# Kernel optimization log

Measured on AMD Instinct MI355X. Metric: run time of the kernel, lower is better.

Reference implementation:

```python
import jax, jax.numpy as jnp
import numpy as np

N_ITEMS = 30000
D = 128            # embedding_dim
F = D // 2 + 1     # freq_dim = 65
RAW_IMG = 1024
RAW_TXT = 768


def setup_inputs() -> dict:
    key = jax.random.key(0)
    ks = jax.random.split(key, 13)
    return {
        "image_embeds": jax.random.normal(ks[0], (N_ITEMS, D), jnp.float32),
        "text_embeds": jax.random.normal(ks[1], (N_ITEMS, D), jnp.float32),
        "image_table": jax.random.normal(ks[2], (N_ITEMS, RAW_IMG), jnp.float32),
        "text_table": jax.random.normal(ks[3], (N_ITEMS, RAW_TXT), jnp.float32),
        "W_img": jax.random.normal(ks[4], (RAW_IMG, D), jnp.float32) * 0.02,
        "b_img": jax.random.normal(ks[5], (D,), jnp.float32) * 0.02,
        "W_txt": jax.random.normal(ks[6], (RAW_TXT, D), jnp.float32) * 0.02,
        "b_txt": jax.random.normal(ks[7], (D,), jnp.float32) * 0.02,
        "avrf_img": jax.random.normal(ks[8], (F,), jnp.float32),
        "avrf_txt": jax.random.normal(ks[9], (F,), jnp.float32),
        "avg_R": jax.random.normal(ks[10], (F,), jnp.float32),
        "psi": jax.random.normal(ks[11], (F,), jnp.float32) * 0.1,
        "lambda_weights": jnp.array([0.6, 0.4], jnp.float32),
    }


def reference(image_embeds, text_embeds, image_table, text_table,
              W_img, b_img, W_txt, b_txt,
              avrf_img, avrf_txt, avg_R, psi, lambda_weights):
    # project full embedding tables: [N, raw] @ [raw, D] -> [N, D]
    proj_image = image_table @ W_img + b_img
    proj_txt = text_table @ W_txt + b_txt
    # per-row rFFT -> [N, F] complex
    img_fft = jnp.fft.rfft(proj_image, axis=1, norm="ortho")
    txt_fft = jnp.fft.rfft(proj_txt, axis=1, norm="ortho")
    # phase alignment rotation
    phi = avg_R * 0.5 + psi                      # [F]
    rot = jnp.exp(-1j * phi.astype(jnp.complex64))
    APC_img = img_fft * rot[None, :]
    APC_txt = txt_fft * jnp.conj(rot)[None, :]
    # AVRF (variance-ratio) masking -- torch forward uses the raw logit params
    img_vr = APC_img * avrf_img[None, :]
    txt_vr = APC_txt * avrf_txt[None, :]
    # IMCF: magnitude-squared coherence masking
    cross = APC_img * jnp.conj(APC_txt)
    msc = jnp.abs(cross) ** 2 / (jnp.abs(APC_img) ** 2 * jnp.abs(APC_txt) ** 2 + 1e-8)
    img_imcf = APC_img * msc
    txt_imcf = APC_txt * msc
    # softmax-weighted late fusion of the two filtered spectra
    lam = jax.nn.softmax(lambda_weights)
    img_late = lam[0] * img_vr + lam[1] * img_imcf
    txt_late = lam[0] * txt_vr + lam[1] * txt_imcf
    image_conv = jnp.fft.irfft(img_late, n=image_embeds.shape[1], axis=1, norm="ortho")
    text_conv = jnp.fft.irfft(txt_late, n=text_embeds.shape[1], axis=1, norm="ortho")
    return image_conv, text_conv
```

## Files before the change

kernel.cpp:

```cpp
#include <hip/hip_runtime.h>
#include <math.h>

typedef __bf16 bf16x8 __attribute__((ext_vector_type(8)));
typedef float f32x4 __attribute__((ext_vector_type(4)));
typedef unsigned short ushort_t;

#define BM 64
#define KS 32
#define S128 0.08838834764831845f
#define TWOPI_128 0.04908738521234052f

__device__ __align__(16) ushort_t g_wft[(32 + 24) * 2 * 6144];
__device__ __align__(16) ushort_t g_gt[6 * 2 * 4096];
__device__ float g_fp[96 * 8];
__device__ unsigned g_spill[512 * 12288];

__device__ __forceinline__ void split2(float v, ushort_t& h, ushort_t& l) {
  unsigned u = __float_as_uint(v);
  h = (ushort_t)(u >> 16);
  float hf = __uint_as_float(u & 0xFFFF0000u);
  float lo = v - hf;
  unsigned ul = __float_as_uint(lo);
  l = (ushort_t)((ul + 0x7FFFu + ((ul >> 16) & 1u)) >> 16);
}

__device__ __forceinline__ void gll16(const void* gsrc, void* ldst) {
  __builtin_amdgcn_global_load_lds(
      (const __attribute__((address_space(1))) unsigned int*)gsrc,
      (__attribute__((address_space(3))) unsigned int*)ldst, 16, 0, 0);
}

__global__ void k_setup_wft(const float* __restrict__ Wimg,
                            const float* __restrict__ Wtxt, int Kimg, int Ktxt) {
  int gid = blockIdx.x * 256 + threadIdx.x;
  int imgn = Kimg * 192;
  if (gid >= imgn + Ktxt * 192) return;
  const float* W;
  int k, c;
  ushort_t* base;
  if (gid < imgn) {
    k = gid / 192; c = gid % 192; W = Wimg + (size_t)k * 128; base = g_wft;
  } else {
    int l = gid - imgn;
    k = l / 192; c = l % 192; W = Wtxt + (size_t)k * 128;
    base = g_wft + (size_t)(Kimg / 32) * 12288;
  }
  int grp = c >> 5, wi = c & 31, part = wi >> 4, fl = grp * 16 + (wi & 15);
  float val = 0.f;
  if (fl <= 64) {
    float re = 0.f, im = 0.f;
    float sts, stc;
    sincosf(TWOPI_128 * (float)fl, &sts, &stc);
    for (int d0 = 0; d0 < 128; d0 += 16) {
      int m = (fl * d0) & 127;
      float sa, ca;
      sincosf(TWOPI_128 * (float)m, &sa, &ca);
      float cr = ca, ci = -sa;
#pragma unroll
      for (int j = 0; j < 16; ++j) {
        float w = W[d0 + j];
        re = fmaf(w, cr, re);
        im = fmaf(w, ci, im);
        float nc = cr * stc + ci * sts;
        ci = ci * stc - cr * sts;
        cr = nc;
      }
    }
    val = (part == 0 ? re : im) * S128;
  }
  ushort_t h, l;
  split2(val, h, l);
  int ks = k >> 5, kin = k & 31;
  base[(size_t)(ks * 2 + 0) * 6144 + c * 32 + kin] = h;
  base[(size_t)(ks * 2 + 1) * 6144 + c * 32 + kin] = l;
}

__global__ void k_setup_gt(void) {
  int gid = blockIdx.x * 256 + threadIdx.x;
  if (gid >= 192 * 128) return;
  int pk = gid >> 7, n = gid & 127;
  int grp = pk >> 5, wi = pk & 31, part = wi >> 4, fl = grp * 16 + (wi & 15);
  float val = 0.f;
  if (fl <= 64) {
    float ck = (fl == 0 || fl == 64) ? 1.f : 2.f;
    int m = (fl * n) & 127;
    float sa, ca;
    sincosf(TWOPI_128 * (float)m, &sa, &ca);
    val = (part == 0 ? ca : -sa) * ck * S128;
  }
  ushort_t h, l;
  split2(val, h, l);
  g_gt[(size_t)(grp * 2 + 0) * 4096 + n * 32 + wi] = h;
  g_gt[(size_t)(grp * 2 + 1) * 4096 + n * 32 + wi] = l;
}

__global__ void k_setup_fp(const float* __restrict__ b_img, const float* __restrict__ b_txt,
                           const float* __restrict__ avrf_img, const float* __restrict__ avrf_txt,
                           const float* __restrict__ avg_R, const float* __restrict__ psi) {
  int gid = blockIdx.x * 256 + threadIdx.x;
  if (gid >= 96 * 4) return;
  int k = gid >> 2, q = gid & 3;
  float* fp = g_fp + k * 8;
  if (k > 64) {
    if (q == 0) { fp[0] = 1.f; fp[1] = 0.f; fp[2] = 0.f; fp[3] = 0.f; }
    fp[4 + q] = 0.f;
    return;
  }
  if (q == 0) {
    float phi = avg_R[k] * 0.5f + psi[k];
    float s, c;
    sincosf(phi, &s, &c);
    fp[0] = c; fp[1] = s; fp[2] = avrf_img[k]; fp[3] = avrf_txt[k];
  }
  const float* b = (q < 2) ? b_img : b_txt;
  int part = q & 1;
  float acc = 0.f;
  for (int d = 0; d < 128; ++d) {
    int m = (k * d) & 127;
    float sa, ca;
    sincosf(TWOPI_128 * (float)m, &sa, &ca);
    acc = fmaf(b[d], part ? -sa : ca, acc);
  }
  fp[4 + q] = acc * S128;
}

__global__ __launch_bounds__(256, 2) void fused_kernel(
    const float* __restrict__ Aimg, const float* __restrict__ Atxt,
    const float* __restrict__ lamw, float* __restrict__ out,
    int M, int Kimg, int Ktxt) {
  __shared__ __align__(16) char smem[67584];
  float* A_lds = (float*)smem;
  ushort_t* B_lds = (ushort_t*)(smem + 16384);
  ushort_t* Yhi = (ushort_t*)smem;
  ushort_t* Ylo = (ushort_t*)(smem + 25600);
  ushort_t* G_lds = (ushort_t*)(smem + 51200);

  const int tid = threadIdx.x, blk = blockIdx.x;
  const int lane = tid & 63, wv = tid >> 6;
  const int la = lane & 15, hh = lane >> 4;
  const int wr = wv >> 1, wc = wv & 1;
  const int row0 = blk * BM;

  f32x4 acc[2][6];

  auto stageA = [&](const float* A, int K, int s, int buf) {
#pragma unroll
    for (int i = 0; i < 2; ++i) {
      int idx = i * 256 + tid;
      int r = idx >> 3, sl = idx & 7;
      int kg = sl ^ (r & 7);
      int grow = row0 + r;
      if (grow > M - 1) grow = M - 1;
      const float* src = A + (size_t)grow * K + s * KS + kg * 4;
      char* dst = (char*)A_lds + buf * 8192 + i * 4096 + wv * 1024;
      gll16(src, dst);
    }
  };
  auto stageB = [&](const ushort_t* wft, int s, int buf) {
#pragma unroll
    for (int i = 0; i < 6; ++i) {
      const ushort_t* src = wft + (size_t)s * 12288 + i * 2048 + tid * 8;
      char* dst = (char*)B_lds + buf * 24576 + i * 4096 + wv * 1024;
      gll16(src, dst);
    }
  };

  auto gemm = [&](const float* A, int K, const ushort_t* wft) {
#pragma unroll
    for (int rt = 0; rt < 2; ++rt)
#pragma unroll
      for (int ct = 0; ct < 6; ++ct) acc[rt][ct] = (f32x4){0.f, 0.f, 0.f, 0.f};
    const int nst = K / KS;
    stageA(A, K, 0, 0);
    stageB(wft, 0, 0);
    for (int s = 0; s < nst; ++s) {
      const int cur = s & 1;
      __syncthreads();
      if (s + 1 < nst) { stageA(A, K, s + 1, cur ^ 1); stageB(wft, s + 1, cur ^ 1); }
      bf16x8 fah[2], fal[2];
#pragma unroll
      for (int rt = 0; rt < 2; ++rt) {
        int row = wr * 32 + rt * 16 + la;
        const float* ab = A_lds + cur * 2048 + row * 32;
        int s0 = (2 * hh) ^ (row & 7);
        int s1 = s0 ^ 1;
        f32x4 q0 = *(const f32x4*)(ab + s0 * 4);
        f32x4 q1 = *(const f32x4*)(ab + s1 * 4);
        ushort_t h8[8], l8[8];
#pragma unroll
        for (int j = 0; j < 4; ++j) {
          split2(q0[j], h8[j], l8[j]);
          split2(q1[j], h8[4 + j], l8[4 + j]);
        }
        fah[rt] = *(bf16x8*)h8;
        fal[rt] = *(bf16x8*)l8;
      }
#pragma unroll
      for (int ct = 0; ct < 6; ++ct) {
        int pcol = wc * 96 + ct * 16 + la;
        const ushort_t* bb = B_lds + cur * 12288 + pcol * 32 + hh * 8;
        bf16x8 fbh = *(const bf16x8*)bb;
        bf16x8 fbl = *(const bf16x8*)(bb + 6144);
#pragma unroll
        for (int rt = 0; rt < 2; ++rt) {
          acc[rt][ct] = __builtin_amdgcn_mfma_f32_16x16x32_bf16(fah[rt], fbh, acc[rt][ct], 0, 0, 0);
          acc[rt][ct] = __builtin_amdgcn_mfma_f32_16x16x32_bf16(fah[rt], fbl, acc[rt][ct], 0, 0, 0);
          acc[rt][ct] = __builtin_amdgcn_mfma_f32_16x16x32_bf16(fal[rt], fbh, acc[rt][ct], 0, 0, 0);
        }
      }
    }
  };

  auto idft = [&](float* outp) {
    f32x4 acc2[2][4];
#pragma unroll
    for (int rt = 0; rt < 2; ++rt)
#pragma unroll
      for (int ct = 0; ct < 4; ++ct) acc2[rt][ct] = (f32x4){0.f, 0.f, 0.f, 0.f};
    for (int ks = 0; ks < 6; ++ks) {
      __syncthreads();
#pragma unroll
      for (int i = 0; i < 4; ++i) {
        const ushort_t* src = g_gt + (size_t)ks * 8192 + i * 2048 + tid * 8;
        char* dst = (char*)G_lds + i * 4096 + wv * 1024;
        gll16(src, dst);
      }
      __syncthreads();
      bf16x8 yah[2], yal[2];
#pragma unroll
      for (int rt = 0; rt < 2; ++rt) {
        int row = wr * 32 + rt * 16 + la;
        int yb = row * 200 + ks * 32 + hh * 8;
        yah[rt] = *(const bf16x8*)&Yhi[yb];
        yal[rt] = *(const bf16x8*)&Ylo[yb];
      }
#pragma unroll
      for (int ct = 0; ct < 4; ++ct) {
        int col = wc * 64 + ct * 16 + la;
        const ushort_t* gb = G_lds + col * 32 + hh * 8;
        bf16x8 gbh = *(const bf16x8*)gb;
        bf16x8 gbl = *(const bf16x8*)(gb + 4096);
#pragma unroll
        for (int rt = 0; rt < 2; ++rt) {
          acc2[rt][ct] = __builtin_amdgcn_mfma_f32_16x16x32_bf16(yah[rt], gbh, acc2[rt][ct], 0, 0, 0);
          acc2[rt][ct] = __builtin_amdgcn_mfma_f32_16x16x32_bf16(yah[rt], gbl, acc2[rt][ct], 0, 0, 0);
          acc2[rt][ct] = __builtin_amdgcn_mfma_f32_16x16x32_bf16(yal[rt], gbh, acc2[rt][ct], 0, 0, 0);
        }
      }
    }
#pragma unroll
    for (int rt = 0; rt < 2; ++rt)
#pragma unroll
      for (int ct = 0; ct < 4; ++ct)
#pragma unroll
        for (int j = 0; j < 4; ++j) {
          int row = row0 + wr * 32 + rt * 16 + hh * 4 + j;
          if (row < M) outp[(size_t)row * 128 + wc * 64 + ct * 16 + la] = acc2[rt][ct][j];
        }
  };

  gemm(Aimg, Kimg, g_wft);
#pragma unroll
  for (int rt = 0; rt < 2; ++rt)
#pragma unroll
    for (int ct = 0; ct < 6; ++ct)
#pragma unroll
      for (int j = 0; j < 4; ++j) {
        ushort_t h, l;
        split2(acc[rt][ct][j], h, l);
        g_spill[(size_t)blk * 12288 + ((rt * 6 + ct) * 4 + j) * 256 + tid] =
            ((unsigned)h << 16) | l;
      }
  gemm(Atxt, Ktxt, g_wft + (size_t)(Kimg / 32) * 12288);
  __syncthreads();

  float l0 = lamw[0], l1 = lamw[1];
  float mx = fmaxf(l0, l1);
  float e0 = expf(l0 - mx), e1 = expf(l1 - mx);
  float lam0 = e0 / (e0 + e1), lam1 = e1 / (e0 + e1);
#pragma unroll
  for (int rt = 0; rt < 2; ++rt)
#pragma unroll
    for (int g = 0; g < 3; ++g) {
      int k = (wc * 3 + g) * 16 + la;
      const float* fp = g_fp + k * 8;
      float rc = fp[0], rs = fp[1], avI = fp[2], avT = fp[3];
      float bIr = fp[4], bIi = fp[5], bTr = fp[6], bTi = fp[7];
#pragma unroll
      for (int j = 0; j < 4; ++j) {
        unsigned uir = g_spill[(size_t)blk * 12288 + ((rt * 6 + 2 * g) * 4 + j) * 256 + tid];
        unsigned uii = g_spill[(size_t)blk * 12288 + ((rt * 6 + 2 * g + 1) * 4 + j) * 256 + tid];
        float Sir = __uint_as_float(uir & 0xFFFF0000u) + __uint_as_float(uir << 16) + bIr;
        float Sii = __uint_as_float(uii & 0xFFFF0000u) + __uint_as_float(uii << 16) + bIi;
        float Str = acc[rt][2 * g][j] + bTr;
        float Sti = acc[rt][2 * g + 1][j] + bTi;
        float Air = Sir * rc + Sii * rs, Aii = Sii * rc - Sir * rs;
        float Atr = Str * rc - Sti * rs, Ati = Sti * rc + Str * rs;
        float cre = Air * Atr + Aii * Ati, cim = Aii * Atr - Air * Ati;
        float pa = Air * Air + Aii * Aii, pb = Atr * Atr + Ati * Ati;
        float msc = (cre * cre + cim * cim) / (pa * pb + 1e-8f);
        float mi = lam0 * avI + lam1 * msc, mt = lam0 * avT + lam1 * msc;
        int row = wr * 32 + rt * 16 + hh * 4 + j;
        int pc = (wc * 3 + g) * 32 + la;
        ushort_t yh, yl;
        split2(Air * mi, yh, yl); Yhi[row * 200 + pc] = yh; Ylo[row * 200 + pc] = yl;
        split2(Aii * mi, yh, yl); Yhi[row * 200 + pc + 16] = yh; Ylo[row * 200 + pc + 16] = yl;
        acc[rt][2 * g][j] = Atr * mt;
        acc[rt][2 * g + 1][j] = Ati * mt;
      }
    }

  idft(out);
  __syncthreads();
#pragma unroll
  for (int rt = 0; rt < 2; ++rt)
#pragma unroll
    for (int g = 0; g < 3; ++g)
#pragma unroll
      for (int j = 0; j < 4; ++j) {
        int row = wr * 32 + rt * 16 + hh * 4 + j;
        int pc = (wc * 3 + g) * 32 + la;
        ushort_t yh, yl;
        split2(acc[rt][2 * g][j], yh, yl);
        Yhi[row * 200 + pc] = yh; Ylo[row * 200 + pc] = yl;
        split2(acc[rt][2 * g + 1][j], yh, yl);
        Yhi[row * 200 + pc + 16] = yh; Ylo[row * 200 + pc + 16] = yl;
      }
  idft(out + (size_t)M * 128);
}

extern "C" void kernel_launch(void* const* d_in, const int* in_sizes, int n_in,
                              void* d_out, int out_size, void* d_ws, size_t ws_size,
                              hipStream_t stream) {
  const float* image_table = (const float*)d_in[2];
  const float* text_table  = (const float*)d_in[3];
  const float* W_img = (const float*)d_in[4];
  const float* b_img = (const float*)d_in[5];
  const float* W_txt = (const float*)d_in[6];
  const float* b_txt = (const float*)d_in[7];
  const float* avrf_img = (const float*)d_in[8];
  const float* avrf_txt = (const float*)d_in[9];
  const float* avg_R = (const float*)d_in[10];
  const float* psi = (const float*)d_in[11];
  const float* lamw = (const float*)d_in[12];

  const int M = in_sizes[0] / 128;
  const int K_img = in_sizes[4] / 128;
  const int K_txt = in_sizes[6] / 128;

  int wft_threads = (K_img + K_txt) * 192;
  k_setup_wft<<<(wft_threads + 255) / 256, 256, 0, stream>>>(W_img, W_txt, K_img, K_txt);
  k_setup_gt<<<(192 * 128 + 255) / 256, 256, 0, stream>>>();
  k_setup_fp<<<2, 256, 0, stream>>>(b_img, b_txt, avrf_img, avrf_txt, avg_R, psi);
  fused_kernel<<<(M + BM - 1) / BM, 256, 0, stream>>>(
      image_table, text_table, lamw, (float*)d_out, M, K_img, K_txt);
}
```

Baseline: 133.6 us.

## Split fused kernel into per-modality GEMM and separate iDFT/filter kernel

Replaces the single fused kernel, which ran image and text GEMMs back to back per block, with a GEMM kernel that launches separate blocks for each modality. This doubles the grid and raises parallelism. The GEMM pre-splits A into bf16 hi/lo once at LDS write time rather than per fragment read. It also changes the weight and iDFT-matrix layouts to 8-element granules and stores the biased spectra to a global buffer. A second kernel reloads both spectra, applies the phase rotation and masks, and runs the inverse DFT for both outputs. The cost is an extra global round trip for the spectra and an extra launch, and the GEMM loop drops LDS double buffering.

```diff
diff --git a/kernel.cpp b/kernel.cpp
--- a/kernel.cpp
+++ b/kernel.cpp
@@ -3,25 +3,25 @@
 
 typedef __bf16 bf16x8 __attribute__((ext_vector_type(8)));
 typedef float f32x4 __attribute__((ext_vector_type(4)));
-typedef unsigned short ushort_t;
-
-#define BM 64
-#define KS 32
+typedef unsigned short u16;
+typedef unsigned int u32;
+
 #define S128 0.08838834764831845f
 #define TWOPI_128 0.04908738521234052f
-
-__device__ __align__(16) ushort_t g_wft[(32 + 24) * 2 * 6144];
-__device__ __align__(16) ushort_t g_gt[6 * 2 * 4096];
-__device__ float g_fp[96 * 8];
-__device__ unsigned g_spill[512 * 12288];
-
-__device__ __forceinline__ void split2(float v, ushort_t& h, ushort_t& l) {
+#define MROWS 30016
+
+__device__ __align__(16) u16 g_wft[56 * 12288];
+__device__ __align__(16) u16 g_gt[6 * 8192];
+__device__ __align__(16) float g_fp[96 * 8];
+__device__ __align__(16) u32 g_S[(size_t)2 * 6 * 4 * MROWS * 8];
+
+__device__ __forceinline__ void split2(float v, u16& h, u16& l) {
   unsigned u = __float_as_uint(v);
-  h = (ushort_t)(u >> 16);
+  h = (u16)(u >> 16);
   float hf = __uint_as_float(u & 0xFFFF0000u);
   float lo = v - hf;
   unsigned ul = __float_as_uint(lo);
-  l = (ushort_t)((ul + 0x7FFFu + ((ul >> 16) & 1u)) >> 16);
+  l = (u16)((ul + 0x7FFFu + ((ul >> 16) & 1u)) >> 16);
 }
 
 __device__ __forceinline__ void gll16(const void* gsrc, void* ldst) {
@@ -33,53 +33,63 @@
 __global__ void k_setup_wft(const float* __restrict__ Wimg,
                             const float* __restrict__ Wtxt, int Kimg, int Ktxt) {
   int gid = blockIdx.x * 256 + threadIdx.x;
-  int imgn = Kimg * 192;
-  if (gid >= imgn + Ktxt * 192) return;
-  const float* W;
-  int k, c;
-  ushort_t* base;
+  int imgn = Kimg * 96;
+  if (gid >= imgn + Ktxt * 96) return;
+  const float* Wrow;
+  u16* base;
+  int kloc, fq;
   if (gid < imgn) {
-    k = gid / 192; c = gid % 192; W = Wimg + (size_t)k * 128; base = g_wft;
+    kloc = gid / 96; fq = gid % 96;
+    Wrow = Wimg + (size_t)kloc * 128;
+    base = g_wft + (size_t)(kloc >> 5) * 12288;
   } else {
     int l = gid - imgn;
-    k = l / 192; c = l % 192; W = Wtxt + (size_t)k * 128;
-    base = g_wft + (size_t)(Kimg / 32) * 12288;
-  }
-  int grp = c >> 5, wi = c & 31, part = wi >> 4, fl = grp * 16 + (wi & 15);
-  float val = 0.f;
-  if (fl <= 64) {
-    float re = 0.f, im = 0.f;
+    kloc = l / 96; fq = l % 96;
+    Wrow = Wtxt + (size_t)kloc * 128;
+    base = g_wft + (size_t)(32 + (kloc >> 5)) * 12288;
+  }
+  float re = 0.f, im = 0.f;
+  if (fq <= 64) {
     float sts, stc;
-    sincosf(TWOPI_128 * (float)fl, &sts, &stc);
+    sincosf(TWOPI_128 * (float)fq, &sts, &stc);
     for (int d0 = 0; d0 < 128; d0 += 16) {
-      int m = (fl * d0) & 127;
+      int m = (fq * d0) & 127;
       float sa, ca;
       sincosf(TWOPI_128 * (float)m, &sa, &ca);
       float cr = ca, ci = -sa;
-#pragma unroll
-      for (int j = 0; j < 16; ++j) {
-        float w = W[d0 + j];
-        re = fmaf(w, cr, re);
-        im = fmaf(w, ci, im);
+      float wv[16];
+      *(float4*)&wv[0]  = *(const float4*)&Wrow[d0];
+      *(float4*)&wv[4]  = *(const float4*)&Wrow[d0 + 4];
+      *(float4*)&wv[8]  = *(const float4*)&Wrow[d0 + 8];
+      *(float4*)&wv[12] = *(const float4*)&Wrow[d0 + 12];
+#pragma unroll
+      for (int jj = 0; jj < 16; ++jj) {
+        re = fmaf(wv[jj], cr, re);
+        im = fmaf(wv[jj], ci, im);
         float nc = cr * stc + ci * sts;
         ci = ci * stc - cr * sts;
         cr = nc;
       }
     }
-    val = (part == 0 ? re : im) * S128;
-  }
-  ushort_t h, l;
-  split2(val, h, l);
-  int ks = k >> 5, kin = k & 31;
-  base[(size_t)(ks * 2 + 0) * 6144 + c * 32 + kin] = h;
-  base[(size_t)(ks * 2 + 1) * 6144 + c * 32 + kin] = l;
+    re *= S128; im *= S128;
+  }
+  int gran = (kloc & 31) >> 3, j = kloc & 7;
+  int cre = (fq >> 4) * 32 + (fq & 15);
+  u16 h, l;
+  split2(re, h, l);
+  base[gran * 1536 + cre * 8 + j] = h;
+  base[6144 + gran * 1536 + cre * 8 + j] = l;
+  split2(im, h, l);
+  base[gran * 1536 + (cre + 16) * 8 + j] = h;
+  base[6144 + gran * 1536 + (cre + 16) * 8 + j] = l;
 }
 
 __global__ void k_setup_gt(void) {
   int gid = blockIdx.x * 256 + threadIdx.x;
   if (gid >= 192 * 128) return;
   int pk = gid >> 7, n = gid & 127;
-  int grp = pk >> 5, wi = pk & 31, part = wi >> 4, fl = grp * 16 + (wi & 15);
+  int ks = pk >> 5, w = pk & 31, gran = (w >> 3) & 3, j = w & 7;
+  int part = w >> 4, fl = ks * 16 + (w & 15);
   float val = 0.f;
   if (fl <= 64) {
     float ck = (fl == 0 || fl == 64) ? 1.f : 2.f;
@@ -88,10 +98,10 @@
     sincosf(TWOPI_128 * (float)m, &sa, &ca);
     val = (part == 0 ? ca : -sa) * ck * S128;
   }
-  ushort_t h, l;
+  u16 h, l;
   split2(val, h, l);
-  g_gt[(size_t)(grp * 2 + 0) * 4096 + n * 32 + wi] = h;
-  g_gt[(size_t)(grp * 2 + 1) * 4096 + n * 32 + wi] = l;
+  g_gt[ks * 8192 + gran * 1024 + n * 8 + j] = h;
+  g_gt[ks * 8192 + 4096 + gran * 1024 + n * 8 + j] = l;
 }
 
 __global__ void k_setup_fp(const float* __restrict__ b_img, const float* __restrict__ b_txt,
@@ -124,209 +134,203 @@
   fp[4 + q] = acc * S128;
 }
 
-__global__ __launch_bounds__(256, 2) void fused_kernel(
+__global__ __launch_bounds__(256) void k1_gemm(
     const float* __restrict__ Aimg, const float* __restrict__ Atxt,
-    const float* __restrict__ lamw, float* __restrict__ out,
-    int M, int Kimg, int Ktxt) {
-  __shared__ __align__(16) char smem[67584];
-  float* A_lds = (float*)smem;
-  ushort_t* B_lds = (ushort_t*)(smem + 16384);
-  ushort_t* Yhi = (ushort_t*)smem;
-  ushort_t* Ylo = (ushort_t*)(smem + 25600);
-  ushort_t* G_lds = (ushort_t*)(smem + 51200);
-
-  const int tid = threadIdx.x, blk = blockIdx.x;
+    int M, int Kimg, int Ktxt, int bpm) {
+  __shared__ __align__(16) u16 Asm[2 * 4096];
+  __shared__ __align__(16) u16 Bsm[2 * 6144];
+
+  const int bid = blockIdx.x;
+  const int mod = bid >= bpm;
+  const int bblk = mod ? bid - bpm : bid;
+  const float* A = mod ? Atxt : Aimg;
+  const int K = mod ? Ktxt : Kimg;
+  const u16* wft = g_wft + (mod ? (size_t)32 * 12288 : 0);
+  const int row0 = bblk * 64;
+
+  const int tid = threadIdx.x;
   const int lane = tid & 63, wv = tid >> 6;
   const int la = lane & 15, hh = lane >> 4;
   const int wr = wv >> 1, wc = wv & 1;
-  const int row0 = blk * BM;
+
+  const int rseg = tid >> 2, kseg = (tid & 3) * 8;
+  int grow = row0 + rseg;
+  if (grow > M - 1) grow = M - 1;
+  const float* Abase = A + (size_t)grow * K + kseg;
 
   f32x4 acc[2][6];
-
-  auto stageA = [&](const float* A, int K, int s, int buf) {
-#pragma unroll
-    for (int i = 0; i < 2; ++i) {
-      int idx = i * 256 + tid;
-      int r = idx >> 3, sl = idx & 7;
-      int kg = sl ^ (r & 7);
-      int grow = row0 + r;
-      if (grow > M - 1) grow = M - 1;
-      const float* src = A + (size_t)grow * K + s * KS + kg * 4;
-      char* dst = (char*)A_lds + buf * 8192 + i * 4096 + wv * 1024;
-      gll16(src, dst);
-    }
-  };
-  auto stageB = [&](const ushort_t* wft, int s, int buf) {
-#pragma unroll
-    for (int i = 0; i < 6; ++i) {
-      const ushort_t* src = wft + (size_t)s * 12288 + i * 2048 + tid * 8;
-      char* dst = (char*)B_lds + buf * 24576 + i * 4096 + wv * 1024;
-      gll16(src, dst);
-    }
-  };
-
-  auto gemm = [&](const float* A, int K, const ushort_t* wft) {
-#pragma unroll
-    for (int rt = 0; rt < 2; ++rt)
-#pragma unroll
-      for (int ct = 0; ct < 6; ++ct) acc[rt][ct] = (f32x4){0.f, 0.f, 0.f, 0.f};
-    const int nst = K / KS;
-    stageA(A, K, 0, 0);
-    stageB(wft, 0, 0);
-    for (int s = 0; s < nst; ++s) {
-      const int cur = s & 1;
-      __syncthreads();
-      if (s + 1 < nst) { stageA(A, K, s + 1, cur ^ 1); stageB(wft, s + 1, cur ^ 1); }
-      bf16x8 fah[2], fal[2];
+#pragma unroll
+  for (int rt = 0; rt < 2; ++rt)
+#pragma unroll
+    for (int ct = 0; ct < 6; ++ct) acc[rt][ct] = (f32x4){0.f, 0.f, 0.f, 0.f};
+
+  const int nst = K / 32;
+  float4 av0 = *(const float4*)(Abase);
+  float4 av1 = *(const float4*)(Abase + 4);
+
+  for (int s = 0; s < nst; ++s) {
+    __syncthreads();
+    {
+      u16 h8[8], l8[8];
+      const float va[8] = {av0.x, av0.y, av0.z, av0.w, av1.x, av1.y, av1.z, av1.w};
+#pragma unroll
+      for (int j = 0; j < 8; ++j) split2(va[j], h8[j], l8[j]);
+      const int ab = (kseg >> 3) * 512 + rseg * 8;
+      *(bf16x8*)&Asm[ab] = *(bf16x8*)h8;
+      *(bf16x8*)&Asm[4096 + ab] = *(bf16x8*)l8;
+    }
+    {
+      const u16* src = wft + (size_t)s * 12288;
+#pragma unroll
+      for (int i = 0; i < 6; ++i)
+        gll16(src + i * 2048 + tid * 8, (char*)Bsm + i * 4096 + tid * 16);
+    }
+    __syncthreads();
+    if (s + 1 < nst) {
+      av0 = *(const float4*)(Abase + (s + 1) * 32);
+      av1 = *(const float4*)(Abase + (s + 1) * 32 + 4);
+    }
+    bf16x8 fah[2], fal[2];
+#pragma unroll
+    for (int rt = 0; rt < 2; ++rt) {
+      const int ar = wr * 32 + rt * 16 + la;
+      fah[rt] = *(const bf16x8*)&Asm[hh * 512 + ar * 8];
+      fal[rt] = *(const bf16x8*)&Asm[4096 + hh * 512 + ar * 8];
+    }
+#pragma unroll
+    for (int ct = 0; ct < 6; ++ct) {
+      const int col = wc * 96 + ct * 16 + la;
+      const u16* bb = &Bsm[hh * 1536 + col * 8];
+      const bf16x8 fbh = *(const bf16x8*)bb;
+      const bf16x8 fbl = *(const bf16x8*)(bb + 6144);
 #pragma unroll
       for (int rt = 0; rt < 2; ++rt) {
-        int row = wr * 32 + rt * 16 + la;
-        const float* ab = A_lds + cur * 2048 + row * 32;
-        int s0 = (2 * hh) ^ (row & 7);
-        int s1 = s0 ^ 1;
-        f32x4 q0 = *(const f32x4*)(ab + s0 * 4);
-        f32x4 q1 = *(const f32x4*)(ab + s1 * 4);
-        ushort_t h8[8], l8[8];
-#pragma unroll
-        for (int j = 0; j < 4; ++j) {
-          split2(q0[j], h8[j], l8[j]);
-          split2(q1[j], h8[4 + j], l8[4 + j]);
-        }
-        fah[rt] = *(bf16x8*)h8;
-        fal[rt] = *(bf16x8*)l8;
+        acc[rt][ct] = __builtin_amdgcn_mfma_f32_16x16x32_bf16(fah[rt], fbh, acc[rt][ct], 0, 0, 0);
+        acc[rt][ct] = __builtin_amdgcn_mfma_f32_16x16x32_bf16(fah[rt], fbl, acc[rt][ct], 0, 0, 0);
+        acc[rt][ct] = __builtin_amdgcn_mfma_f32_16x16x32_bf16(fal[rt], fbh, acc[rt][ct], 0, 0, 0);
       }
-#pragma unroll
-      for (int ct = 0; ct < 6; ++ct) {
-        int pcol = wc * 96 + ct * 16 + la;
-        const ushort_t* bb = B_lds + cur * 12288 + pcol * 32 + hh * 8;
-        bf16x8 fbh = *(const bf16x8*)bb;
-        bf16x8 fbl = *(const bf16x8*)(bb + 6144);
-#pragma unroll
-        for (int rt = 0; rt < 2; ++rt) {
-          acc[rt][ct] = __builtin_amdgcn_mfma_f32_16x16x32_bf16(fah[rt], fbh, acc[rt][ct], 0, 0, 0);
-          acc[rt][ct] = __builtin_amdgcn_mfma_f32_16x16x32_bf16(fah[rt], fbl, acc[rt][ct], 0, 0, 0);
-          acc[rt][ct] = __builtin_amdgcn_mfma_f32_16x16x32_bf16(fal[rt], fbh, acc[rt][ct], 0, 0, 0);
-        }
+    }
+  }
+
+#pragma unroll
+  for (int ct = 0; ct < 6; ++ct) {
+    const int cg = wc * 6 + ct;
+    const int fq = (cg >> 1) * 16 + la;
+    const float bv = g_fp[fq * 8 + 4 + mod * 2 + (cg & 1)];
+    const int ks = cg >> 1;
+    const int khh = (cg & 1) * 2 + (la >> 3);
+    const int j8 = la & 7;
+    const size_t sbase = ((size_t)((mod * 6 + ks) * 4 + khh)) * MROWS;
+#pragma unroll
+    for (int rt = 0; rt < 2; ++rt) {
+      const int rb = row0 + wr * 32 + rt * 16 + hh * 4;
+#pragma unroll
+      for (int j = 0; j < 4; ++j) {
+        u16 h, l;
+        split2(acc[rt][ct][j] + bv, h, l);
+        g_S[(sbase + rb + j) * 8 + j8] = ((u32)h << 16) | l;
       }
     }
-  };
-
-  auto idft = [&](float* outp) {
-    f32x4 acc2[2][4];
-#pragma unroll
-    for (int rt = 0; rt < 2; ++rt)
-#pragma unroll
-      for (int ct = 0; ct < 4; ++ct) acc2[rt][ct] = (f32x4){0.f, 0.f, 0.f, 0.f};
-    for (int ks = 0; ks < 6; ++ks) {
-      __syncthreads();
-#pragma unroll
-      for (int i = 0; i < 4; ++i) {
-        const ushort_t* src = g_gt + (size_t)ks * 8192 + i * 2048 + tid * 8;
-        char* dst = (char*)G_lds + i * 4096 + wv * 1024;
-        gll16(src, dst);
+  }
+}
+
+__global__ __launch_bounds__(256) void k2_idft(
+    const float* __restrict__ lamw, float* __restrict__ out, int M) {
+  __shared__ __align__(16) u16 Gs[8192];
+  __shared__ __align__(16) float fps[96 * 8];
+
+  const int tid = threadIdx.x;
+  const int lane = tid & 63, wv = tid >> 6;
+  const int la = lane & 15, hh = lane >> 4;
+  const int part = hh >> 1;
+  const int row = blockIdx.x * 64 + wv * 16 + la;
+
+  if (tid < 192) gll16((const char*)g_fp + tid * 16, (char*)fps + tid * 16);
+
+  const float l0 = lamw[0], l1 = lamw[1];
+  const float mx = fmaxf(l0, l1);
+  const float e0 = expf(l0 - mx), e1 = expf(l1 - mx);
+  const float lam0 = e0 / (e0 + e1), lam1 = e1 / (e0 + e1);
+
+  f32x4 ai[8], at[8];
+#pragma unroll
+  for (int ct = 0; ct < 8; ++ct) {
+    ai[ct] = (f32x4){0.f, 0.f, 0.f, 0.f};
+    at[ct] = (f32x4){0.f, 0.f, 0.f, 0.f};
+  }
+
+  for (int ks = 0; ks < 6; ++ks) {
+    const u32* si = &g_S[((size_t)((0 + ks) * 4 + hh) * MROWS + row) * 8];
+    const u32* st = &g_S[((size_t)((24 + ks * 4) + hh) * MROWS + row) * 8];
+    uint4 vi0 = *(const uint4*)si, vi1 = *(const uint4*)(si + 4);
+    uint4 vt0 = *(const uint4*)st, vt1 = *(const uint4*)(st + 4);
+
+    __syncthreads();
+#pragma unroll
+    for (int i = 0; i < 4; ++i)
+      gll16((const char*)(g_gt + ks * 8192) + i * 4096 + tid * 16,
+            (char*)Gs + i * 4096 + tid * 16);
+    __syncthreads();
+
+    u32 vs_i[8], vs_t[8];
+    *(uint4*)&vs_i[0] = vi0; *(uint4*)&vs_i[4] = vi1;
+    *(uint4*)&vs_t[0] = vt0; *(uint4*)&vs_t[4] = vt1;
+
+    const int fq0 = ks * 16 + (hh & 1) * 8;
+    u16 yih[8], yil[8], yth[8], ytl[8];
+#pragma unroll
+    for (int j = 0; j < 8; ++j) {
+      const f32x4 fpv = *(const f32x4*)&fps[(fq0 + j) * 8];
+      const float o_i = __uint_as_float(vs_i[j] & 0xFFFF0000u) + __uint_as_float(vs_i[j] << 16);
+      const float o_t = __uint_as_float(vs_t[j] & 0xFFFF0000u) + __uint_as_float(vs_t[j] << 16);
+      const float p_i = __shfl_xor(o_i, 32);
+      const float p_t = __shfl_xor(o_t, 32);
+      const float Sre_i = part ? p_i : o_i;
+      const float Sim_i = part ? o_i : p_i;
+      const float Sre_t = part ? p_t : o_t;
+      const float Sim_t = part ? o_t : p_t;
+      const float rc = fpv[0], rs = fpv[1];
+      const float Air = Sre_i * rc + Sim_i * rs, Aii = Sim_i * rc - Sre_i * rs;
+      const float Atr = Sre_t * rc - Sim_t * rs, Ati = Sim_t * rc + Sre_t * rs;
+      const float cre = Air * Atr + Aii * Ati, cim = Aii * Atr - Air * Ati;
+      const float pa = Air * Air + Aii * Aii, pb = Atr * Atr + Ati * Ati;
+      const float msc = (cre * cre + cim * cim) / (pa * pb + 1e-8f);
+      const float mi = lam0 * fpv[2] + lam1 * msc;
+      const float mt = lam0 * fpv[3] + lam1 * msc;
+      const float yi = (part ? Aii : Air) * mi;
+      const float yt = (part ? Ati : Atr) * mt;
+      split2(yi, yih[j], yil[j]);
+      split2(yt, yth[j], ytl[j]);
+    }
+    const bf16x8 fih = *(bf16x8*)yih, fil = *(bf16x8*)yil;
+    const bf16x8 fth = *(bf16x8*)yth, ftl = *(bf16x8*)ytl;
+#pragma unroll
+    for (int ct = 0; ct < 8; ++ct) {
+      const u16* gb = &Gs[hh * 1024 + (ct * 16 + la) * 8];
+      const bf16x8 gh = *(const bf16x8*)gb;
+      const bf16x8 gl = *(const bf16x8*)(gb + 4096);
+      ai[ct] = __builtin_amdgcn_mfma_f32_16x16x32_bf16(fih, gh, ai[ct], 0, 0, 0);
+      ai[ct] = __builtin_amdgcn_mfma_f32_16x16x32_bf16(fih, gl, ai[ct], 0, 0, 0);
+      ai[ct] = __builtin_amdgcn_mfma_f32_16x16x32_bf16(fil, gh, ai[ct], 0, 0, 0);
+      at[ct] = __builtin_amdgcn_mfma_f32_16x16x32_bf16(fth, gh, at[ct], 0, 0, 0);
+      at[ct] = __builtin_amdgcn_mfma_f32_16x16x32_bf16(fth, gl, at[ct], 0, 0, 0);
+      at[ct] = __builtin_amdgcn_mfma_f32_16x16x32_bf16(ftl, gh, at[ct], 0, 0, 0);
+    }
+  }
+
+  float* oimg = out;
+  float* otxt = out + (size_t)M * 128;
+#pragma unroll
+  for (int q = 0; q < 4; ++q) {
+    const int orow = blockIdx.x * 64 + wv * 16 + hh * 4 + q;
+    if (orow < M) {
+#pragma unroll
+      for (int ct = 0; ct < 8; ++ct) {
+        oimg[(size_t)orow * 128 + ct * 16 + la] = ai[ct][q];
+        otxt[(size_t)orow * 128 + ct * 16 + la] = at[ct][q];
       }
-      __syncthreads();
-      bf16x8 yah[2], yal[2];
-#pragma unroll
-      for (int rt = 0; rt < 2; ++rt) {
-        int row = wr * 32 + rt * 16 + la;
-        int yb = row * 200 + ks * 32 + hh * 8;
-        yah[rt] = *(const bf16x8*)&Yhi[yb];
-        yal[rt] = *(const bf16x8*)&Ylo[yb];
-      }
-#pragma unroll
-      for (int ct = 0; ct < 4; ++ct) {
-        int col = wc * 64 + ct * 16 + la;
-        const ushort_t* gb = G_lds + col * 32 + hh * 8;
-        bf16x8 gbh = *(const bf16x8*)gb;
-        bf16x8 gbl = *(const bf16x8*)(gb + 4096);
-#pragma unroll
-        for (int rt = 0; rt < 2; ++rt) {
-          acc2[rt][ct] = __builtin_amdgcn_mfma_f32_16x16x32_bf16(yah[rt], gbh, acc2[rt][ct], 0, 0, 0);
-          acc2[rt][ct] = __builtin_amdgcn_mfma_f32_16x16x32_bf16(yah[rt], gbl, acc2[rt][ct], 0, 0, 0);
-          acc2[rt][ct] = __builtin_amdgcn_mfma_f32_16x16x32_bf16(yal[rt], gbh, acc2[rt][ct], 0, 0, 0);
-        }
-      }
-    }
-#pragma unroll
-    for (int rt = 0; rt < 2; ++rt)
-#pragma unroll
-      for (int ct = 0; ct < 4; ++ct)
-#pragma unroll
-        for (int j = 0; j < 4; ++j) {
-          int row = row0 + wr * 32 + rt * 16 + hh * 4 + j;
-          if (row < M) outp[(size_t)row * 128 + wc * 64 + ct * 16 + la] = acc2[rt][ct][j];
-        }
-  };
-
-  gemm(Aimg, Kimg, g_wft);
-#pragma unroll
-  for (int rt = 0; rt < 2; ++rt)
-#pragma unroll
-    for (int ct = 0; ct < 6; ++ct)
-#pragma unroll
-      for (int j = 0; j < 4; ++j) {
-        ushort_t h, l;
-        split2(acc[rt][ct][j], h, l);
-        g_spill[(size_t)blk * 12288 + ((rt * 6 + ct) * 4 + j) * 256 + tid] =
-            ((unsigned)h << 16) | l;
-      }
-  gemm(Atxt, Ktxt, g_wft + (size_t)(Kimg / 32) * 12288);
-  __syncthreads();
-
-  float l0 = lamw[0], l1 = lamw[1];
-  float mx = fmaxf(l0, l1);
-  float e0 = expf(l0 - mx), e1 = expf(l1 - mx);
-  float lam0 = e0 / (e0 + e1), lam1 = e1 / (e0 + e1);
-#pragma unroll
-  for (int rt = 0; rt < 2; ++rt)
-#pragma unroll
-    for (int g = 0; g < 3; ++g) {
-      int k = (wc * 3 + g) * 16 + la;
-      const float* fp = g_fp + k * 8;
-      float rc = fp[0], rs = fp[1], avI = fp[2], avT = fp[3];
-      float bIr = fp[4], bIi = fp[5], bTr = fp[6], bTi = fp[7];
-#pragma unroll
-      for (int j = 0; j < 4; ++j) {
-        unsigned uir = g_spill[(size_t)blk * 12288 + ((rt * 6 + 2 * g) * 4 + j) * 256 + tid];
-        unsigned uii = g_spill[(size_t)blk * 12288 + ((rt * 6 + 2 * g + 1) * 4 + j) * 256 + tid];
-        float Sir = __uint_as_float(uir & 0xFFFF0000u) + __uint_as_float(uir << 16) + bIr;
-        float Sii = __uint_as_float(uii & 0xFFFF0000u) + __uint_as_float(uii << 16) + bIi;
-        float Str = acc[rt][2 * g][j] + bTr;
-        float Sti = acc[rt][2 * g + 1][j] + bTi;
-        float Air = Sir * rc + Sii * rs, Aii = Sii * rc - Sir * rs;
-        float Atr = Str * rc - Sti * rs, Ati = Sti * rc + Str * rs;
-        float cre = Air * Atr + Aii * Ati, cim = Aii * Atr - Air * Ati;
-        float pa = Air * Air + Aii * Aii, pb = Atr * Atr + Ati * Ati;
-        float msc = (cre * cre + cim * cim) / (pa * pb + 1e-8f);
-        float mi = lam0 * avI + lam1 * msc, mt = lam0 * avT + lam1 * msc;
-        int row = wr * 32 + rt * 16 + hh * 4 + j;
-        int pc = (wc * 3 + g) * 32 + la;
-        ushort_t yh, yl;
-        split2(Air * mi, yh, yl); Yhi[row * 200 + pc] = yh; Ylo[row * 200 + pc] = yl;
-        split2(Aii * mi, yh, yl); Yhi[row * 200 + pc + 16] = yh; Ylo[row * 200 + pc + 16] = yl;
-        acc[rt][2 * g][j] = Atr * mt;
-        acc[rt][2 * g + 1][j] = Ati * mt;
-      }
-    }
-
-  idft(out);
-  __syncthreads();
-#pragma unroll
-  for (int rt = 0; rt < 2; ++rt)
-#pragma unroll
-    for (int g = 0; g < 3; ++g)
-#pragma unroll
-      for (int j = 0; j < 4; ++j) {
-        int row = wr * 32 + rt * 16 + hh * 4 + j;
-        int pc = (wc * 3 + g) * 32 + la;
-        ushort_t yh, yl;
-        split2(acc[rt][2 * g][j], yh, yl);
-        Yhi[row * 200 + pc] = yh; Ylo[row * 200 + pc] = yl;
-        split2(acc[rt][2 * g + 1][j], yh, yl);
-        Yhi[row * 200 + pc + 16] = yh; Ylo[row * 200 + pc + 16] = yl;
-      }
-  idft(out + (size_t)M * 128);
+    }
+  }
 }
 
 extern "C" void kernel_launch(void* const* d_in, const int* in_sizes, int n_in,
@@ -348,10 +352,12 @@
   const int K_img = in_sizes[4] / 128;
   const int K_txt = in_sizes[6] / 128;
 
-  int wft_threads = (K_img + K_txt) * 192;
+  const int wft_threads = (K_img + K_txt) * 96;
   k_setup_wft<<<(wft_threads + 255) / 256, 256, 0, stream>>>(W_img, W_txt, K_img, K_txt);
   k_setup_gt<<<(192 * 128 + 255) / 256, 256, 0, stream>>>();
   k_setup_fp<<<2, 256, 0, stream>>>(b_img, b_txt, avrf_img, avrf_txt, avg_R, psi);
-  fused_kernel<<<(M + BM - 1) / BM, 256, 0, stream>>>(
-      image_table, text_table, lamw, (float*)d_out, M, K_img, K_txt);
-}
+
+  const int bpm = (M + 63) / 64;
+  k1_gemm<<<2 * bpm, 256, 0, stream>>>(image_table, text_table, M, K_img, K_txt, bpm);
+  k2_idft<<<bpm, 256, 0, stream>>>(lamw, (float*)d_out, M);
+}
```

Result: slower. 149.5 us (+11.9%).
